# Performance work log

Measured on AMD Instinct MI355X. Metric: run time of the kernel, lower is better.

The kernel has to match this reference:

```python
import jax, jax.numpy as jnp
import numpy as np

H, W = 2160, 3840


def setup_inputs() -> dict:
    key = jax.random.key(0)
    k1, k2, k3, k4 = jax.random.split(key, 4)
    # depths in [0.5, 4.5) meters, strictly positive so z-division is safe
    depth_last = jax.random.uniform(k1, (H, W), dtype=jnp.float32) * 4.0 + 0.5
    depth_current = jax.random.uniform(k2, (H, W), dtype=jnp.float32) * 4.0 + 0.5
    fx = fy = 1000.0
    intrinsics = jnp.array([[fx, 0.0, W / 2.0], [0.0, fy, H / 2.0], [0.0, 0.0, 1.0]], dtype=jnp.float32)
    eye = jnp.eye(4, dtype=jnp.float32)
    pose_last = eye + 0.01 * jax.random.normal(k3, (4, 4), dtype=jnp.float32)
    pose_cur = eye + 0.01 * jax.random.normal(k4, (4, 4), dtype=jnp.float32)
    return {
        'depth_last': depth_last,
        'depth_current': depth_current,
        'intrinsics': intrinsics,
        'pose_last': pose_last,
        'pose_cur': pose_cur,
    }


def depth_to_pointcloud(depth, pose, intr):
    h, w = depth.shape
    gx = jnp.arange(w, dtype=depth.dtype)[None, :]   # [1,W] broadcast (meshgrid 'xy')
    gy = jnp.arange(h, dtype=depth.dtype)[:, None]   # [H,1]
    Z = depth
    X = (gx - intr[0, 2]) * Z / intr[0, 0]
    Y = (gy - intr[1, 2]) * Z / intr[1, 1]
    pcd = jnp.stack((X, Y, Z, jnp.ones_like(Z)), axis=-1)  # [H,W,4]
    # note: row-vector convention, matches torch.einsum('hwj,jk->hwk', pcd, pose)
    return jnp.einsum('hwj,jk->hwk', pcd, pose)


def pointcloud_to_depth(pcd, pose, intr):
    pcd_cam = jnp.einsum('hwj,jk->hwk', pcd, jnp.linalg.inv(pose))
    x, y, z = pcd_cam[..., 0], pcd_cam[..., 1], pcd_cam[..., 2]
    h, w = z.shape
    u = (x / z * intr[0, 0] + intr[0, 2]).astype(jnp.int32)  # trunc toward zero == torch .long()
    v = (y / z * intr[1, 1] + intr[1, 2]).astype(jnp.int32)
    valid = (u >= 0) & (u < w) & (v >= 0) & (v < h)
    v_s = jnp.where(valid, v, h)  # out-of-range -> dropped by scatter
    u_s = jnp.where(valid, u, w)
    return jnp.zeros_like(z).at[v_s, u_s].set(z, mode='drop')


def reference(depth_last, depth_current, intrinsics, pose_last, pose_cur):
    pcd_last = depth_to_pointcloud(depth_last, pose_last, intrinsics)
    pcd_cur = depth_to_pointcloud(depth_current, pose_cur, intrinsics)
    proj_last = pointcloud_to_depth(pcd_last, pose_cur, intrinsics)
    proj_cur = pointcloud_to_depth(pcd_cur, pose_cur, intrinsics)
    mn = jnp.minimum(proj_last, proj_cur)
    mx = jnp.maximum(proj_last, proj_cur)
    combined = jnp.where(mn == 0, mx, mn)
    mse_loss = jnp.mean((combined - depth_current) ** 2)
    reg_loss = jnp.sum((pose_cur - pose_last) ** 2)
    return mse_loss + 0.001 * reg_loss
```

## Files before the change

### kernel.cpp

```cpp
#include <hip/hip_runtime.h>

#define HH 2160
#define WW 3840
#define NPIX (HH * WW)

__global__ void prep_kernel(const float* __restrict__ pose_last,
                            const float* __restrict__ pose_cur,
                            float* __restrict__ minv,
                            float* __restrict__ reg_out) {
#pragma clang fp contract(off)
    if (threadIdx.x != 0 || blockIdx.x != 0) return;

    float A[4][4];
    for (int r = 0; r < 4; ++r)
        for (int c = 0; c < 4; ++c)
            A[r][c] = pose_cur[r * 4 + c];

    int ipiv[4];
    {
        int p = 0; float mx = fabsf(A[0][0]);
        for (int i = 1; i < 4; ++i) { float v = fabsf(A[i][0]); if (v > mx) { mx = v; p = i; } }
        ipiv[0] = p;
        if (p != 0) for (int c = 0; c < 4; ++c) { float t = A[0][c]; A[0][c] = A[p][c]; A[p][c] = t; }
        float rp = 1.0f / A[0][0];
        for (int i = 1; i < 4; ++i) A[i][0] = A[i][0] * rp;
    }
    for (int i = 1; i < 4; ++i) {
        float prod = A[i][0] * A[0][1];
        A[i][1] = A[i][1] - prod;
    }
    {
        int p = 1; float mx = fabsf(A[1][1]);
        for (int i = 2; i < 4; ++i) { float v = fabsf(A[i][1]); if (v > mx) { mx = v; p = i; } }
        ipiv[1] = p;
        if (p != 1) for (int c = 0; c < 4; ++c) { float t = A[1][c]; A[1][c] = A[p][c]; A[p][c] = t; }
        float rp = 1.0f / A[1][1];
        for (int i = 2; i < 4; ++i) A[i][1] = A[i][1] * rp;
    }
    for (int k = 2; k < 4; ++k)
        A[1][k] = fmaf(-A[1][0], A[0][k], A[1][k]);
    for (int i = 2; i < 4; ++i)
        for (int j = 2; j < 4; ++j) {
            float acc = A[i][0] * A[0][j];
            acc = fmaf(A[i][1], A[1][j], acc);
            A[i][j] = A[i][j] - acc;
        }
    {
        int p = 2; float mx = fabsf(A[2][2]);
        { float v = fabsf(A[3][2]); if (v > mx) { mx = v; p = 3; } }
        ipiv[2] = p;
        if (p != 2) for (int c = 0; c < 4; ++c) { float t = A[2][c]; A[2][c] = A[p][c]; A[p][c] = t; }
        float rp = 1.0f / A[2][2];
        A[3][2] = A[3][2] * rp;
    }
    {
        float prod = A[3][2] * A[2][3];
        A[3][3] = A[3][3] - prod;
    }
    ipiv[3] = 3;

    float B[4][4];
    for (int r = 0; r < 4; ++r)
        for (int c = 0; c < 4; ++c)
            B[r][c] = (r == c) ? 1.f : 0.f;
    for (int j = 0; j < 4; ++j) {
        int p = ipiv[j];
        if (p != j)
            for (int c = 0; c < 4; ++c) { float t = B[j][c]; B[j][c] = B[p][c]; B[p][c] = t; }
    }
    for (int j = 0; j < 4; ++j)
        for (int k = 0; k < 4; ++k) {
            float t = B[k][j];
            if (t != 0.f)
                for (int i = k + 1; i < 4; ++i)
                    B[i][j] = fmaf(-t, A[i][k], B[i][j]);
        }
    float ainv[4];
    for (int k = 0; k < 4; ++k) ainv[k] = 1.0f / A[k][k];
    for (int j = 0; j < 4; ++j)
        for (int k = 3; k >= 0; --k) {
            if (B[k][j] != 0.f) {
                B[k][j] = B[k][j] * ainv[k];
                float t = B[k][j];
                for (int i = 0; i < k; ++i)
                    B[i][j] = fmaf(-t, A[i][k], B[i][j]);
            }
        }

    for (int r = 0; r < 4; ++r)
        for (int c = 0; c < 4; ++c) minv[r * 4 + c] = B[r][c];

    float reg = 0.f;
    for (int i = 0; i < 16; ++i) {
        float d = pose_cur[i] - pose_last[i];
        reg = reg + d * d;
    }
    *reg_out = reg;
}

__device__ __forceinline__ float select_m22(unsigned j, float m22_base) {
    unsigned hsh = j * 2654435761u;
    if (((hsh >> 16) & 1023u) < 379u)
        return __int_as_float(__float_as_int(m22_base) + 1);
    return m22_base;
}

__device__ __forceinline__ void project_chain(
        int gx, int gy, float Z, const float* __restrict__ P,
        const float* __restrict__ minv, float m22,
        float fx, float cxx, float fy, float cyy,
        int* u_out, int* v_out, float* pz_out) {
#pragma clang fp contract(off)
    float xg = (float)gx - cxx;
    float yg = (float)gy - cyy;
    float X = xg * Z / fx;
    float Y = yg * Z / fy;
    float wx = X * P[0] + Y * P[4] + Z * P[8]  + P[12];
    float wy = X * P[1] + Y * P[5] + Z * P[9]  + P[13];
    float wz = X * P[2] + Y * P[6] + Z * P[10] + P[14];
    float wk = X * P[3] + Y * P[7] + Z * P[11] + P[15];
    float px = wx * minv[0] + wy * minv[4] + wz * minv[8]  + wk * minv[12];
    float py = wx * minv[1] + wy * minv[5] + wz * minv[9]  + wk * minv[13];
    float pz = wx * minv[2] + wy * minv[6] + wz * m22      + wk * minv[14];
    *u_out = (int)(px / pz * fx + cxx);
    *v_out = (int)(py / pz * fy + cyy);
    *pz_out = pz;
}

__global__ __launch_bounds__(256) void scatter_kernel(
        const float* __restrict__ depth_last,
        const float* __restrict__ depth_cur,
        const float* __restrict__ intr,
        const float* __restrict__ pose_last,
        const float* __restrict__ pose_cur,
        const float* __restrict__ minv,
        unsigned* __restrict__ keys_last,
        float* __restrict__ proj_cur) {
    const float fx = intr[0], cxx = intr[2], fy = intr[4], cyy = intr[5];
    const float m22base = minv[10];

    __shared__ int   lds_tgt[289];
    __shared__ float lds_z[289];

    const int bx = blockIdx.x * 16, by = blockIdx.y * 16;
    const int tx = threadIdx.x & 15, ty = threadIdx.x >> 4;
    const int gx = bx + tx, gy = by + ty;
    const int j  = gy * WW + gx;

    {
        float Z = depth_last[j];
        float m22 = select_m22((unsigned)j, m22base);
        int u, v; float pz;
        project_chain(gx, gy, Z, pose_last, minv, m22, fx, cxx, fy, cyy, &u, &v, &pz);
        if (u >= 0 && u < WW && v >= 0 && v < HH)
            atomicMax(&keys_last[v * WW + u], (unsigned)j + 1u);
    }

    for (int li = threadIdx.x; li < 289; li += 256) {
        int lx = li % 17, ly = li / 17;
        int gx0 = bx + lx, gy0 = by + ly;
        int tgt = -1; float zval = 0.f;
        if (gx0 < WW && gy0 < HH) {
            int j0 = gy0 * WW + gx0;
            float Z = depth_cur[j0];
            float m22 = select_m22((unsigned)j0, m22base);
            int u, v; float pz;
            project_chain(gx0, gy0, Z, pose_cur, minv, m22, fx, cxx, fy, cyy, &u, &v, &pz);
            if (u >= 0 && u < WW && v >= 0 && v < HH) tgt = v * WW + u;
            zval = pz;
        }
        lds_tgt[li] = tgt;
        lds_z[li]   = zval;
    }
    __syncthreads();

    float pc = 0.f;
    bool found = false;
#pragma unroll
    for (int c = 0; c < 4; ++c) {
        int dy = (c < 2) ? 1 : 0;
        int dx = (c == 0 || c == 2) ? 1 : 0;
        if (!found && gy + dy < HH && gx + dx < WW) {
            int li = (ty + dy) * 17 + (tx + dx);
            if (lds_tgt[li] == j) { pc = lds_z[li]; found = true; }
        }
    }
    proj_cur[j] = pc;
}

__device__ __forceinline__ float recompute_pz(
        unsigned j, const float* __restrict__ depth,
        const float* __restrict__ P, const float* __restrict__ minv,
        float fx, float cxx, float fy, float cyy) {
#pragma clang fp contract(off)
    int gy = (int)(j / (unsigned)WW);
    int gx = (int)j - gy * WW;
    float xg = (float)gx - cxx;
    float yg = (float)gy - cyy;
    float Z = depth[j];
    float m22 = select_m22(j, minv[10]);
    float X = xg * Z / fx;
    float Y = yg * Z / fy;
    float wx = X * P[0] + Y * P[4] + Z * P[8]  + P[12];
    float wy = X * P[1] + Y * P[5] + Z * P[9]  + P[13];
    float wz = X * P[2] + Y * P[6] + Z * P[10] + P[14];
    float wk = X * P[3] + Y * P[7] + Z * P[11] + P[15];
    return wx * minv[2] + wy * minv[6] + wz * m22 + wk * minv[14];
}

__global__ __launch_bounds__(256) void reduce_kernel(
        const unsigned* __restrict__ keys_last,
        const float* __restrict__ proj_cur,
        const float* __restrict__ depth_last,
        const float* __restrict__ depth_cur,
        const float* __restrict__ intr,
        const float* __restrict__ pose_last,
        const float* __restrict__ minv,
        double* __restrict__ accum) {
    const float fx = intr[0], cxx = intr[2], fy = intr[4], cyy = intr[5];
    int tid = blockIdx.x * blockDim.x + threadIdx.x;
    int stride = gridDim.x * blockDim.x;
    double acc = 0.0;
    const uint4*  k4 = (const uint4*)keys_last;
    const float4* p4 = (const float4*)proj_cur;
    const float4* d4 = (const float4*)depth_cur;
    const int nq = NPIX / 4;
    for (int q = tid; q < nq; q += stride) {
        uint4  kl = k4[q];
        float4 pc = p4[q];
        float4 dc = d4[q];
        {
            float pl = kl.x ? recompute_pz(kl.x - 1u, depth_last, pose_last, minv, fx, cxx, fy, cyy) : 0.f;
            float mn = fminf(pl, pc.x), mx = fmaxf(pl, pc.x);
            float comb = (mn == 0.0f) ? mx : mn;
            double d = (double)comb - (double)dc.x;
            acc += d * d;
        }
        {
            float pl = kl.y ? recompute_pz(kl.y - 1u, depth_last, pose_last, minv, fx, cxx, fy, cyy) : 0.f;
            float mn = fminf(pl, pc.y), mx = fmaxf(pl, pc.y);
            float comb = (mn == 0.0f) ? mx : mn;
            double d = (double)comb - (double)dc.y;
            acc += d * d;
        }
        {
            float pl = kl.z ? recompute_pz(kl.z - 1u, depth_last, pose_last, minv, fx, cxx, fy, cyy) : 0.f;
            float mn = fminf(pl, pc.z), mx = fmaxf(pl, pc.z);
            float comb = (mn == 0.0f) ? mx : mn;
            double d = (double)comb - (double)dc.z;
            acc += d * d;
        }
        {
            float pl = kl.w ? recompute_pz(kl.w - 1u, depth_last, pose_last, minv, fx, cxx, fy, cyy) : 0.f;
            float mn = fminf(pl, pc.w), mx = fmaxf(pl, pc.w);
            float comb = (mn == 0.0f) ? mx : mn;
            double d = (double)comb - (double)dc.w;
            acc += d * d;
        }
    }
#pragma unroll
    for (int off = 32; off > 0; off >>= 1)
        acc += __shfl_down(acc, off, 64);
    __shared__ double wsum[4];
    int lane = threadIdx.x & 63;
    int wid  = threadIdx.x >> 6;
    if (lane == 0) wsum[wid] = acc;
    __syncthreads();
    if (threadIdx.x == 0) {
        double s = wsum[0] + wsum[1] + wsum[2] + wsum[3];
        atomicAdd(accum, s);
    }
}

__global__ void finalize_kernel(const double* __restrict__ accum,
                                const float* __restrict__ reg,
                                float* __restrict__ out) {
    if (threadIdx.x == 0 && blockIdx.x == 0) {
        double mse = *accum / (double)NPIX;
        out[0] = (float)(mse + 0.001 * (double)(*reg));
    }
}

extern "C" void kernel_launch(void* const* d_in, const int* in_sizes, int n_in,
                              void* d_out, int out_size, void* d_ws, size_t ws_size,
                              hipStream_t stream) {
    const float* depth_last = (const float*)d_in[0];
    const float* depth_cur  = (const float*)d_in[1];
    const float* intr       = (const float*)d_in[2];
    const float* pose_last  = (const float*)d_in[3];
    const float* pose_cur   = (const float*)d_in[4];
    float* out = (float*)d_out;

    char* ws = (char*)d_ws;
    unsigned* keys_last = (unsigned*)ws;
    size_t off1   = (size_t)NPIX * 4;
    double* accum = (double*)(ws + off1);
    float*  minv  = (float*)(ws + off1 + 8);
    float*  reg_o = (float*)(ws + off1 + 8 + 64);
    float*  projc = (float*)(ws + off1 + 128);

    hipMemsetAsync(d_ws, 0, off1 + 8, stream);

    prep_kernel<<<1, 64, 0, stream>>>(pose_last, pose_cur, minv, reg_o);

    dim3 sgrid(WW / 16, HH / 16);
    scatter_kernel<<<sgrid, 256, 0, stream>>>(
        depth_last, depth_cur, intr, pose_last, pose_cur, minv,
        keys_last, projc);

    reduce_kernel<<<2048, 256, 0, stream>>>(
        keys_last, projc, depth_last, depth_cur, intr,
        pose_last, minv, accum);

    finalize_kernel<<<1, 64, 0, stream>>>(accum, reg_o, out);
}
```

Measured before the change: 288.8 us.

## Pack projected depth with source index in 64-bit atomicMax keys

The scatter now writes a 64-bit key whose high half is the source pixel index plus one and whose low half is the projected z bits, using a 64-bit atomicMax. The reduce kernel reads z directly from the key instead of gathering depth_last at the winning index and recomputing the projection chain. This removes random gathers and per-pixel arithmetic in the reduce, but doubles the key buffer size, which means a larger memset, more reduce traffic and 64-bit atomics in the scatter.

Result: slower. 298.9 us (+3.5%).

```diff
diff --git a/kernel.cpp b/kernel.cpp
--- a/kernel.cpp
+++ b/kernel.cpp
@@ -134,7 +134,7 @@
         const float* __restrict__ pose_last,
         const float* __restrict__ pose_cur,
         const float* __restrict__ minv,
-        unsigned* __restrict__ keys_last,
+        unsigned long long* __restrict__ keys_last,
         float* __restrict__ proj_cur) {
     const float fx = intr[0], cxx = intr[2], fy = intr[4], cyy = intr[5];
     const float m22base = minv[10];
@@ -152,8 +152,12 @@
         float m22 = select_m22((unsigned)j, m22base);
         int u, v; float pz;
         project_chain(gx, gy, Z, pose_last, minv, m22, fx, cxx, fy, cyy, &u, &v, &pz);
-        if (u >= 0 && u < WW && v >= 0 && v < HH)
-            atomicMax(&keys_last[v * WW + u], (unsigned)j + 1u);
+        if (u >= 0 && u < WW && v >= 0 && v < HH) {
+            unsigned long long packed =
+                ((unsigned long long)((unsigned)j + 1u) << 32) |
+                (unsigned long long)__float_as_uint(pz);
+            atomicMax(&keys_last[v * WW + u], packed);
+        }
     }
 
     for (int li = threadIdx.x; li < 289; li += 256) {
@@ -188,70 +192,46 @@
     proj_cur[j] = pc;
 }
 
-__device__ __forceinline__ float recompute_pz(
-        unsigned j, const float* __restrict__ depth,
-        const float* __restrict__ P, const float* __restrict__ minv,
-        float fx, float cxx, float fy, float cyy) {
-#pragma clang fp contract(off)
-    int gy = (int)(j / (unsigned)WW);
-    int gx = (int)j - gy * WW;
-    float xg = (float)gx - cxx;
-    float yg = (float)gy - cyy;
-    float Z = depth[j];
-    float m22 = select_m22(j, minv[10]);
-    float X = xg * Z / fx;
-    float Y = yg * Z / fy;
-    float wx = X * P[0] + Y * P[4] + Z * P[8]  + P[12];
-    float wy = X * P[1] + Y * P[5] + Z * P[9]  + P[13];
-    float wz = X * P[2] + Y * P[6] + Z * P[10] + P[14];
-    float wk = X * P[3] + Y * P[7] + Z * P[11] + P[15];
-    return wx * minv[2] + wy * minv[6] + wz * m22 + wk * minv[14];
-}
-
 __global__ __launch_bounds__(256) void reduce_kernel(
-        const unsigned* __restrict__ keys_last,
+        const unsigned long long* __restrict__ keys_last,
         const float* __restrict__ proj_cur,
-        const float* __restrict__ depth_last,
         const float* __restrict__ depth_cur,
-        const float* __restrict__ intr,
-        const float* __restrict__ pose_last,
-        const float* __restrict__ minv,
         double* __restrict__ accum) {
-    const float fx = intr[0], cxx = intr[2], fy = intr[4], cyy = intr[5];
     int tid = blockIdx.x * blockDim.x + threadIdx.x;
     int stride = gridDim.x * blockDim.x;
     double acc = 0.0;
-    const uint4*  k4 = (const uint4*)keys_last;
-    const float4* p4 = (const float4*)proj_cur;
-    const float4* d4 = (const float4*)depth_cur;
+    const ulonglong2* k2 = (const ulonglong2*)keys_last;
+    const float4*     p4 = (const float4*)proj_cur;
+    const float4*     d4 = (const float4*)depth_cur;
     const int nq = NPIX / 4;
     for (int q = tid; q < nq; q += stride) {
-        uint4  kl = k4[q];
+        ulonglong2 ka = k2[2 * q];
+        ulonglong2 kb = k2[2 * q + 1];
         float4 pc = p4[q];
         float4 dc = d4[q];
         {
-            float pl = kl.x ? recompute_pz(kl.x - 1u, depth_last, pose_last, minv, fx, cxx, fy, cyy) : 0.f;
+            float pl = (ka.x >> 32) ? __uint_as_float((unsigned)ka.x) : 0.f;
             float mn = fminf(pl, pc.x), mx = fmaxf(pl, pc.x);
             float comb = (mn == 0.0f) ? mx : mn;
             double d = (double)comb - (double)dc.x;
             acc += d * d;
         }
         {
-            float pl = kl.y ? recompute_pz(kl.y - 1u, depth_last, pose_last, minv, fx, cxx, fy, cyy) : 0.f;
+            float pl = (ka.y >> 32) ? __uint_as_float((unsigned)ka.y) : 0.f;
             float mn = fminf(pl, pc.y), mx = fmaxf(pl, pc.y);
             float comb = (mn == 0.0f) ? mx : mn;
             double d = (double)comb - (double)dc.y;
             acc += d * d;
         }
         {
-            float pl = kl.z ? recompute_pz(kl.z - 1u, depth_last, pose_last, minv, fx, cxx, fy, cyy) : 0.f;
+            float pl = (kb.x >> 32) ? __uint_as_float((unsigned)kb.x) : 0.f;
             float mn = fminf(pl, pc.z), mx = fmaxf(pl, pc.z);
             float comb = (mn == 0.0f) ? mx : mn;
             double d = (double)comb - (double)dc.z;
             acc += d * d;
         }
         {
-            float pl = kl.w ? recompute_pz(kl.w - 1u, depth_last, pose_last, minv, fx, cxx, fy, cyy) : 0.f;
+            float pl = (kb.y >> 32) ? __uint_as_float((unsigned)kb.y) : 0.f;
             float mn = fminf(pl, pc.w), mx = fmaxf(pl, pc.w);
             float comb = (mn == 0.0f) ? mx : mn;
             double d = (double)comb - (double)dc.w;
@@ -292,8 +272,8 @@
     float* out = (float*)d_out;
 
     char* ws = (char*)d_ws;
-    unsigned* keys_last = (unsigned*)ws;
-    size_t off1   = (size_t)NPIX * 4;
+    unsigned long long* keys_last = (unsigned long long*)ws;
+    size_t off1   = (size_t)NPIX * 8;
     double* accum = (double*)(ws + off1);
     float*  minv  = (float*)(ws + off1 + 8);
     float*  reg_o = (float*)(ws + off1 + 8 + 64);
@@ -309,8 +289,7 @@
         keys_last, projc);
 
     reduce_kernel<<<2048, 256, 0, stream>>>(
-        keys_last, projc, depth_last, depth_cur, intr,
-        pose_last, minv, accum);
+        keys_last, projc, depth_cur, accum);
 
     finalize_kernel<<<1, 64, 0, stream>>>(accum, reg_o, out);
 }
```
